# Performance work log

Hardware: AMD Instinct MI355X
Metric: run time of the kernel (lower is better)

Reference implementation:

```python
import jax, jax.numpy as jnp
import numpy as np

T, B, N, M, H, I = 64, 256, 256, 128, 1024, 128
S = 3  # 2*shift_range + 1
EPS = 1e-8  # torch cosine_similarity eps


def setup_inputs() -> dict:
    key = jax.random.key(0)
    ks = jax.random.split(key, 24)
    def rn(k, shp, scale):
        return (jax.random.normal(k, shp) * scale).astype(jnp.float32)
    sH = 1.0 / np.sqrt(H)
    sC = 1.0 / np.sqrt(I + M)
    sM = 1.0 / np.sqrt(M)
    return {
        'x': rn(ks[0], (T, B, I), 1.0),
        # controller (ffnn): Linear(I+M -> H), stored as [in, out]
        'Wc': rn(ks[1], (I + M, H), sC), 'bc': jnp.zeros((H,), jnp.float32),
        # head params stacked: index 0 = write head, 1 = read head
        'Wk': rn(ks[2], (2, H, M), sH), 'bk': jnp.zeros((2, M), jnp.float32),
        'Wb': rn(ks[3], (2, H, 1), sH), 'bb': jnp.zeros((2, 1), jnp.float32),
        'Wg': rn(ks[4], (2, H, 1), sH), 'bg': jnp.zeros((2, 1), jnp.float32),
        'Ws': rn(ks[5], (2, H, S), sH), 'bs': jnp.zeros((2, S), jnp.float32),
        'Wgam': rn(ks[6], (2, H, 1), sH), 'bgam': jnp.zeros((2, 1), jnp.float32),
        'We': rn(ks[7], (H, M), sH), 'be': jnp.zeros((M,), jnp.float32),
        'Wa': rn(ks[8], (H, M), sH), 'ba': rn(ks[9], (M,), 1.0),
        'Wo': rn(ks[10], (M, I), sM), 'bo': jnp.zeros((I,), jnp.float32),
        # learned initial state
        'memory0': rn(ks[11], (1, N, M), 0.05),
        'ww0': rn(ks[12], (1, N), 0.05),
        'rw0': rn(ks[13], (1, N), 0.05),
        'read0': rn(ks[14], (1, M), 0.05),
    }


def reference(x, Wc, bc, Wk, bk, Wb, bb, Wg, bg, Ws, bs, Wgam, bgam,
              We, be, Wa, ba, Wo, bo, memory0, ww0, rw0, read0):
    Bb = x.shape[1]
    Nn = memory0.shape[1]

    def head(i, ht, memory, prev_w):
        k = jax.nn.relu(ht @ Wk[i] + bk[i])                      # [B, M]
        beta = jax.nn.softplus(ht @ Wb[i] + bb[i])               # [B, 1]
        g = jax.nn.sigmoid(ht @ Wg[i] + bg[i])                   # [B, 1]
        shift = jax.nn.softmax(ht @ Ws[i] + bs[i], axis=1)       # [B, S]
        gamma = jax.nn.relu(ht @ Wgam[i] + bgam[i]) + 1.0        # [B, 1]
        # content addressing: cosine similarity then sharpened softmax
        kn = jnp.maximum(jnp.linalg.norm(k, axis=-1, keepdims=True), EPS)   # [B,1]
        mn = jnp.maximum(jnp.linalg.norm(memory, axis=-1), EPS)             # [B,N]
        cos = jnp.einsum('bm,bnm->bn', k, memory) / (kn * mn)
        w = jax.nn.softmax(beta * cos, axis=1)
        # interpolation with previous weight
        w = g * w + (1.0 - g) * prev_w
        # circular convolutional shift (kernel size S=3, cross-correlation like F.conv1d)
        pad = jnp.concatenate([w[:, -1:], w, w[:, :1]], axis=1)  # [B, N+2]
        w = sum(shift[:, j:j + 1] * pad[:, j:j + Nn] for j in range(S))
        # sharpening
        w = w ** gamma
        return w / jnp.sum(w, axis=1, keepdims=True)

    mem = jnp.tile(memory0, (Bb, 1, 1))
    ww = jax.nn.softmax(jnp.tile(ww0, (Bb, 1)), axis=1)
    rw = jax.nn.softmax(jnp.tile(rw0, (Bb, 1)), axis=1)
    rd = jnp.tile(read0, (Bb, 1))

    def step(carry, xt):
        memory, ww, rw, rd = carry
        inp = jnp.concatenate([xt, rd], axis=1)
        ht = jnp.tanh(inp @ Wc + bc)                             # ffnn controller
        ww = head(0, ht, memory, ww)                             # write head
        rw = head(1, ht, memory, rw)                             # read head
        erase = jax.nn.sigmoid(ht @ We + be)                     # [B, M]
        add = jax.nn.sigmoid(ht @ Wa + ba)                       # [B, M]
        memory = memory * (1.0 - ww[:, :, None] * erase[:, None, :]) \
                 + ww[:, :, None] * add[:, None, :]
        rd = jnp.einsum('bn,bnm->bm', rw, memory)
        out = rd @ Wo + bo
        return (memory, ww, rw, rd), out

    _, ys = jax.lax.scan(step, (mem, ww, rw, rd), x)
    return ys  # [T, B, I]
```

## Files before the change

kernel.cpp:

```cpp
#include <hip/hip_runtime.h>
#include <math.h>

#define T_ 64
#define B_ 256
#define N_ 256
#define M_ 128
#define H_ 1024
#define I_ 128
#define NB 256
#define NT 1024
#define MSTR 132
#define EPSF 1e-8f

#define WS_WCX 0
#define WS_WCR 65536
#define WS_W2P 131072
#define WS_WOP 393216
#define WS_WSM 401408
#define WS_XC  407552
#define WS_BYTES_NEEDED ((size_t)(407552 + 8388608) * 4)

typedef _Float16 h2_t __attribute__((ext_vector_type(2)));

__device__ __forceinline__ float fdot2(unsigned a, unsigned b, float c) {
  union { unsigned u; h2_t h; } ua, ub;
  ua.u = a; ub.u = b;
  return __builtin_amdgcn_fdot2(ua.h, ub.h, c, false);
}
__device__ __forceinline__ unsigned packh2(float a, float b) {
  union { h2_t h; unsigned u; } v;
  v.h = h2_t{(_Float16)a, (_Float16)b};
  return v.u;
}
__device__ __forceinline__ float dot4(uint4 w, uint4 h, float acc) {
  acc = fdot2(w.x, h.x, acc); acc = fdot2(w.y, h.y, acc);
  acc = fdot2(w.z, h.z, acc); acc = fdot2(w.w, h.w, acc);
  return acc;
}
__device__ __forceinline__ float wave_rsum(float v) {
#pragma unroll
  for (int o = 32; o > 0; o >>= 1) v += __shfl_xor(v, o, 64);
  return v;
}
__device__ __forceinline__ float wave_rmax(float v) {
#pragma unroll
  for (int o = 32; o > 0; o >>= 1) v = fmaxf(v, __shfl_xor(v, o, 64));
  return v;
}

__global__ void ntm_pack(const float* __restrict__ Wc, const float* __restrict__ Wk,
                         const float* __restrict__ Wb, const float* __restrict__ Wg,
                         const float* __restrict__ Wsf, const float* __restrict__ Wgm,
                         const float* __restrict__ We, const float* __restrict__ Wa,
                         const float* __restrict__ Wo,
                         unsigned* __restrict__ wsu)
{
  const int total = 407552;
  for (int i = blockIdx.x * blockDim.x + threadIdx.x; i < total;
       i += gridDim.x * blockDim.x) {
    if (i < 65536) {
      int jm = i & 3, q4 = i >> 2, k4 = q4 >> 10, h = q4 & 1023;
      int k0 = k4 * 8 + 2 * jm;
      wsu[WS_WCX + i] = packh2(Wc[(size_t)k0 * H_ + h], Wc[(size_t)(k0 + 1) * H_ + h]);
    } else if (i < 131072) {
      int u = i - 65536;
      int jm = u & 3, q4 = u >> 2, k4 = q4 >> 10, h = q4 & 1023;
      int k0 = 128 + k4 * 8 + 2 * jm;
      wsu[WS_WCR + u] = packh2(Wc[(size_t)k0 * H_ + h], Wc[(size_t)(k0 + 1) * H_ + h]);
    } else if (i < 393216) {
      int u = i - 131072;
      int jm = u & 3, q4 = u >> 2, k4 = q4 >> 9, c = q4 & 511;
      int k0 = k4 * 8 + 2 * jm, k1 = k0 + 1;
      float v0, v1;
      if (c < 128)      { v0 = Wk[(size_t)k0 * M_ + c];           v1 = Wk[(size_t)k1 * M_ + c]; }
      else if (c < 256) { v0 = Wk[(size_t)H_ * M_ + (size_t)k0 * M_ + (c - 128)];
                          v1 = Wk[(size_t)H_ * M_ + (size_t)k1 * M_ + (c - 128)]; }
      else if (c < 384) { v0 = We[(size_t)k0 * M_ + (c - 256)];   v1 = We[(size_t)k1 * M_ + (c - 256)]; }
      else              { v0 = Wa[(size_t)k0 * M_ + (c - 384)];   v1 = Wa[(size_t)k1 * M_ + (c - 384)]; }
      wsu[WS_W2P + u] = packh2(v0, v1);
    } else if (i < 401408) {
      int u = i - 393216;
      int jm = u & 3, q4 = u >> 2, k4 = q4 >> 7, c = q4 & 127;
      int m0 = k4 * 8 + 2 * jm;
      wsu[WS_WOP + u] = packh2(Wo[(size_t)m0 * I_ + c], Wo[(size_t)(m0 + 1) * I_ + c]);
    } else {
      int u = i - 401408, d = u >> 9, k2 = u & 511;
      int k0 = 2 * k2, k1 = 2 * k2 + 1;
      float v0, v1;
      if (d < 2)      { v0 = Wb[d * H_ + k0];        v1 = Wb[d * H_ + k1]; }
      else if (d < 4) { v0 = Wg[(d - 2) * H_ + k0];  v1 = Wg[(d - 2) * H_ + k1]; }
      else if (d < 6) { v0 = Wgm[(d - 4) * H_ + k0]; v1 = Wgm[(d - 4) * H_ + k1]; }
      else if (d < 9) { v0 = Wsf[k0 * 3 + (d - 6)];  v1 = Wsf[k1 * 3 + (d - 6)]; }
      else            { v0 = Wsf[3 * H_ + k0 * 3 + (d - 9)]; v1 = Wsf[3 * H_ + k1 * 3 + (d - 9)]; }
      wsu[WS_WSM + u] = packh2(v0, v1);
    }
  }
}

__global__ __launch_bounds__(256)
void ntm_xc(const float* __restrict__ x, const unsigned* __restrict__ wsu,
            unsigned* __restrict__ wsout)
{
  __shared__ __align__(16) _Float16 xt[16 * 128];
  const int tid = threadIdx.x;
  const size_t row0 = (size_t)blockIdx.x * 16;
  for (int i = tid; i < 16 * 128; i += 256)
    xt[i] = (_Float16)x[(row0 + (i >> 7)) * I_ + (i & 127)];
  __syncthreads();
  _Float16* xc16 = (_Float16*)(wsout + WS_XC);
  const uint4* xt4 = (const uint4*)xt;
  const uint4* w4 = (const uint4*)(wsu + WS_WCX);
  for (int cq = 0; cq < 4; ++cq) {
    const int col = cq * 256 + tid;
    float acc[16];
#pragma unroll
    for (int r = 0; r < 16; ++r) acc[r] = 0.f;
#pragma unroll 4
    for (int k4 = 0; k4 < 16; ++k4) {
      uint4 w = w4[k4 * 1024 + col];
#pragma unroll
      for (int r = 0; r < 16; ++r)
        acc[r] = dot4(w, xt4[r * 16 + k4], acc[r]);
    }
#pragma unroll
    for (int r = 0; r < 16; ++r)
      xc16[(row0 + r) * H_ + col] = (_Float16)acc[r];
  }
}

__global__ __launch_bounds__(NT)
void ntm_main(const float* __restrict__ x,
              const float* __restrict__ bc,  const float* __restrict__ bk,
              const float* __restrict__ bbv, const float* __restrict__ bg,
              const float* __restrict__ bsf, const float* __restrict__ bgm,
              const float* __restrict__ be,  const float* __restrict__ ba,
              const float* __restrict__ bo,
              const float* __restrict__ mem0, const float* __restrict__ ww0,
              const float* __restrict__ rw0,  const float* __restrict__ rd0,
              const unsigned* __restrict__ wsu,
              float* __restrict__ out, int useXc)
{
  __shared__ __align__(16) float mem[N_ * MSTR];
  __shared__ __align__(16) _Float16 ht16[H_];
  __shared__ __align__(16) _Float16 rd16[M_];
  __shared__ __align__(16) _Float16 x16[M_];
  __shared__ __align__(16) float prevw[2 * N_];
  __shared__ __align__(16) float mnv[N_];
  __shared__ __align__(16) float ksh[2 * M_];
  __shared__ __align__(16) float eah[2 * M_];
  __shared__ __align__(16) float wlog[2 * N_];
  __shared__ __align__(16) float wtmp[2 * N_];
  __shared__ __align__(16) float redU[2048];
  __shared__ __align__(16) float sdots[24];
  __shared__ __align__(16) float scal[32];
  __shared__ __align__(16) float bcL[H_];
  __shared__ __align__(16) float bkL[256];
  __shared__ __align__(16) float beL[128];
  __shared__ __align__(16) float baL[128];
  __shared__ __align__(16) float boL[128];
  __shared__ __align__(16) float sb[16];

  const int tid = threadIdx.x;
  const int b = blockIdx.x;
  const _Float16* xcg = (const _Float16*)(wsu + WS_XC);
  const uint4* wcx4 = (const uint4*)(wsu + WS_WCX);
  const uint4* wcr4 = (const uint4*)(wsu + WS_WCR);
  const uint4* w2p4 = (const uint4*)(wsu + WS_W2P);
  const uint4* wop4 = (const uint4*)(wsu + WS_WOP);
  const uint4* wsm4 = (const uint4*)(wsu + WS_WSM);
  const uint4* rp4 = (const uint4*)rd16;
  const uint4* hp4 = (const uint4*)ht16;

  for (int i = tid; i < N_ * M_; i += NT)
    mem[(i >> 7) * MSTR + (i & 127)] = mem0[i];
  bcL[tid] = bc[tid];
  if (tid < 256) bkL[tid] = bk[tid];
  if (tid < 128) { beL[tid] = be[tid]; baL[tid] = ba[tid]; boL[tid] = bo[tid]; }
  if (tid < 12) {
    float v;
    if (tid < 2) v = bbv[tid];
    else if (tid < 4) v = bg[tid - 2];
    else if (tid < 6) v = bgm[tid - 4];
    else v = bsf[tid - 6];
    sb[tid] = v;
  }
  if (tid < 512) wlog[tid] = (tid < 256) ? ww0[tid] : rw0[tid - 256];
  __syncthreads();
  if (tid < 256) {
    float s = 0.f;
#pragma unroll 8
    for (int m = 0; m < M_; ++m) { float v = mem[tid * MSTR + m]; s += v * v; }
    mnv[tid] = fmaxf(sqrtf(s), EPSF);
  }
  {
    int wv = tid >> 6, ln = tid & 63;
    if (wv < 2) {
      float l0 = wlog[wv * N_ + ln], l1 = wlog[wv * N_ + 64 + ln],
            l2 = wlog[wv * N_ + 128 + ln], l3 = wlog[wv * N_ + 192 + ln];
      float mx = wave_rmax(fmaxf(fmaxf(l0, l1), fmaxf(l2, l3)));
      float e0 = __expf(l0 - mx), e1 = __expf(l1 - mx), e2 = __expf(l2 - mx), e3 = __expf(l3 - mx);
      float sm = wave_rsum(e0 + e1 + e2 + e3);
      wlog[wv * N_ + ln] = e0; wlog[wv * N_ + 64 + ln] = e1;
      wlog[wv * N_ + 128 + ln] = e2; wlog[wv * N_ + 192 + ln] = e3;
      if (ln == 0) scal[30 + wv] = 1.f / sm;
    }
  }
  __syncthreads();
  if (tid < 512) prevw[tid] = wlog[tid] * scal[30 + (tid >> 8)];
  if (tid < 64)
    ((unsigned*)rd16)[tid] = packh2(rd0[2 * tid], rd0[2 * tid + 1]);
  if (!useXc && tid >= 64 && tid < 128) {
    int k = tid - 64;
    ((unsigned*)x16)[k] = packh2(x[(size_t)b * I_ + 2 * k], x[(size_t)b * I_ + 2 * k + 1]);
  }
  __syncthreads();

  for (int t = 0; t < T_; ++t) {
    {
      const int j = tid;
      float a0, a1 = 0.f;
      if (useXc) {
        a0 = (float)xcg[((size_t)t * B_ + b) * H_ + j];
      } else {
        a0 = 0.f;
        const uint4* xp4 = (const uint4*)x16;
#pragma unroll 4
        for (int k4 = 0; k4 < 16; k4 += 2) {
          a0 = dot4(wcx4[k4 * 1024 + j], xp4[k4], a0);
          a1 = dot4(wcx4[(k4 + 1) * 1024 + j], xp4[k4 + 1], a1);
        }
      }
#pragma unroll 4
      for (int k4 = 0; k4 < 16; k4 += 2) {
        a0 = dot4(wcr4[k4 * 1024 + j], rp4[k4], a0);
        a1 = dot4(wcr4[(k4 + 1) * 1024 + j], rp4[k4 + 1], a1);
      }
      ht16[j] = (_Float16)tanhf(a0 + a1 + bcL[j]);
      if (t > 0) {
        int c = tid & 127, q = tid >> 7;
        float s = dot4(wop4[(2 * q) * 128 + c], rp4[2 * q], 0.f);
        s = dot4(wop4[(2 * q + 1) * 128 + c], rp4[2 * q + 1], s);
        redU[1024 + q * 128 + c] = s;
      }
    }
    __syncthreads();

    {
      const int c = tid & 511, half = tid >> 9;
      const int kb = half * 64;
      float a0 = 0.f, a1 = 0.f, a2 = 0.f, a3 = 0.f;
#pragma unroll 8
      for (int k = 0; k < 64; k += 4) {
        a0 = dot4(w2p4[(kb + k) * 512 + c],     hp4[kb + k],     a0);
        a1 = dot4(w2p4[(kb + k + 1) * 512 + c], hp4[kb + k + 1], a1);
        a2 = dot4(w2p4[(kb + k + 2) * 512 + c], hp4[kb + k + 2], a2);
        a3 = dot4(w2p4[(kb + k + 3) * 512 + c], hp4[kb + k + 3], a3);
      }
      redU[half * 512 + c] = (a0 + a1) + (a2 + a3);
      if (tid < 128 && t > 0) {
        float o = boL[tid];
#pragma unroll
        for (int q = 0; q < 8; ++q) o += redU[1024 + q * 128 + tid];
        out[((size_t)(t - 1) * B_ + b) * I_ + tid] = o;
      }
    }
    __syncthreads();

    {
      if (tid < 512) {
        float v = redU[tid] + redU[512 + tid];
        if (tid < 256)      ksh[tid] = fmaxf(v + bkL[tid], 0.f);
        else if (tid < 384) eah[tid - 256] = 1.f / (1.f + __expf(-(v + beL[tid - 256])));
        else                eah[tid - 256] = 1.f / (1.f + __expf(-(v + baL[tid - 384])));
      } else {
        int wv = (tid >> 6) - 8, ln = tid & 63;
#pragma unroll
        for (int i = 0; i < 3; ++i) {
          int hd = wv * 3 + i;
          int d = hd >> 1, half = hd & 1;
          float s = dot4(wsm4[d * 128 + half * 64 + ln], hp4[half * 64 + ln], 0.f);
          s = wave_rsum(s);
          if (ln == 0) sdots[hd] = s;
        }
      }
    }
    __syncthreads();

    {
      if (tid == 0) {
        for (int h = 0; h < 2; ++h) {
          float Sb = sdots[2 * h] + sdots[2 * h + 1];
          float Sg = sdots[2 * (2 + h)] + sdots[2 * (2 + h) + 1];
          float Sgm = sdots[2 * (4 + h)] + sdots[2 * (4 + h) + 1];
          float rb = Sb + sb[h];
          scal[16 + h] = (rb > 20.f) ? rb : log1pf(__expf(rb));
          scal[18 + h] = 1.f / (1.f + __expf(-(Sg + sb[2 + h])));
          scal[20 + h] = fmaxf(Sgm + sb[4 + h], 0.f) + 1.f;
          float s0 = sdots[2 * (6 + 3 * h)] + sdots[2 * (6 + 3 * h) + 1] + sb[6 + 3 * h];
          float s1 = sdots[2 * (7 + 3 * h)] + sdots[2 * (7 + 3 * h) + 1] + sb[7 + 3 * h];
          float s2 = sdots[2 * (8 + 3 * h)] + sdots[2 * (8 + 3 * h) + 1] + sb[8 + 3 * h];
          float mx = fmaxf(s0, fmaxf(s1, s2));
          float e0 = __expf(s0 - mx), e1 = __expf(s1 - mx), e2 = __expf(s2 - mx);
          float inv = 1.f / (e0 + e1 + e2);
          scal[22 + 3 * h] = e0 * inv; scal[23 + 3 * h] = e1 * inv; scal[24 + 3 * h] = e2 * inv;
        }
      } else if (tid >= 64 && tid < 192) {
        int h = (tid >> 6) - 1, ln = tid & 63;
        float v0 = ksh[h * 128 + ln], v1 = ksh[h * 128 + 64 + ln];
        float s = wave_rsum(v0 * v0 + v1 * v1);
        if (ln == 0) scal[12 + h] = fmaxf(sqrtf(s), EPSF);
      }
    }
    __syncthreads();

    if (tid < 512) {
      int wv = tid >> 6, ln = tid & 63;
      int h = wv & 1, n = (wv >> 1) * 64 + ln;
      const float beta = scal[16 + h], kn = scal[12 + h];
      const float4* kp = (const float4*)&ksh[h * 128];
      const float* mrow = &mem[n * MSTR];
      float dot = 0.f;
#pragma unroll 8
      for (int m4 = 0; m4 < 32; ++m4) {
        float4 kv = kp[m4];
        float4 mv = *(const float4*)&mrow[m4 * 4];
        dot += kv.x * mv.x + kv.y * mv.y + kv.z * mv.z + kv.w * mv.w;
      }
      wlog[h * N_ + n] = beta * (dot / (kn * mnv[n]));
    }
    __syncthreads();

    {
      int wv = tid >> 6, ln = tid & 63;
      if (wv < 2) {
        float l0 = wlog[wv * N_ + ln], l1 = wlog[wv * N_ + 64 + ln],
              l2 = wlog[wv * N_ + 128 + ln], l3 = wlog[wv * N_ + 192 + ln];
        float mx = wave_rmax(fmaxf(fmaxf(l0, l1), fmaxf(l2, l3)));
        float e0 = __expf(l0 - mx), e1 = __expf(l1 - mx), e2 = __expf(l2 - mx), e3 = __expf(l3 - mx);
        float sm = wave_rsum(e0 + e1 + e2 + e3);
        wlog[wv * N_ + ln] = e0; wlog[wv * N_ + 64 + ln] = e1;
        wlog[wv * N_ + 128 + ln] = e2; wlog[wv * N_ + 192 + ln] = e3;
        if (ln == 0) scal[30 + wv] = 1.f / sm;
      }
    }
    __syncthreads();

    if (tid < 512) {
      int h = tid >> 8;
      float g = scal[18 + h];
      wtmp[tid] = g * wlog[tid] * scal[30 + h] + (1.f - g) * prevw[tid];
    }
    __syncthreads();

    if (tid < 512) {
      int h = tid >> 8, n = tid & 255;
      float v = scal[22 + 3 * h] * wtmp[h * N_ + ((n + 255) & 255)]
              + scal[23 + 3 * h] * wtmp[h * N_ + n]
              + scal[24 + 3 * h] * wtmp[h * N_ + ((n + 1) & 255)];
      wlog[tid] = __powf(v, scal[20 + h]);
    }
    __syncthreads();

    {
      int wv = tid >> 6, ln = tid & 63;
      if (wv < 2) {
        float s = wlog[wv * N_ + ln] + wlog[wv * N_ + 64 + ln]
                + wlog[wv * N_ + 128 + ln] + wlog[wv * N_ + 192 + ln];
        s = wave_rsum(s);
        if (ln == 0) scal[14 + wv] = 1.f / s;
      }
    }
    __syncthreads();

    {
      int n = tid & 255, q = tid >> 8;
      float wwn = wlog[n] * scal[14];
      float* mrow = &mem[n * MSTR + q * 32];
      const float4* ep = (const float4*)&eah[q * 32];
      const float4* ap = (const float4*)&eah[128 + q * 32];
      float sq = 0.f;
#pragma unroll
      for (int i = 0; i < 8; ++i) {
        float4 mv = *(float4*)&mrow[i * 4];
        float4 ev = ep[i], av = ap[i];
        mv.x = mv.x * (1.f - wwn * ev.x) + wwn * av.x;
        mv.y = mv.y * (1.f - wwn * ev.y) + wwn * av.y;
        mv.z = mv.z * (1.f - wwn * ev.z) + wwn * av.z;
        mv.w = mv.w * (1.f - wwn * ev.w) + wwn * av.w;
        sq += mv.x * mv.x + mv.y * mv.y + mv.z * mv.z + mv.w * mv.w;
        *(float4*)&mrow[i * 4] = mv;
      }
      redU[1024 + q * 256 + n] = sq;
      if (q == 0) prevw[n] = wwn;
    }
    __syncthreads();

    {
      int m = tid & 127, g = tid >> 7;
      const float* basep = &mem[g * 32 * MSTR + m];
      float acc = 0.f;
#pragma unroll 8
      for (int i = 0; i < 32; ++i)
        acc += wlog[256 + g * 32 + i] * basep[i * MSTR];
      redU[g * 128 + m] = acc;
    }
    __syncthreads();

    {
      if (tid < 64) {
        float r0 = 0.f, r1 = 0.f;
#pragma unroll
        for (int g = 0; g < 8; ++g) {
          r0 += redU[g * 128 + 2 * tid];
          r1 += redU[g * 128 + 2 * tid + 1];
        }
        ((unsigned*)rd16)[tid] = packh2(r0 * scal[15], r1 * scal[15]);
      } else if (tid >= 256 && tid < 512) {
        int n = tid - 256;
        prevw[256 + n] = wlog[256 + n] * scal[15];
      } else if (tid >= 512 && tid < 768) {
        int n = tid - 512;
        float s = redU[1024 + n] + redU[1280 + n] + redU[1536 + n] + redU[1792 + n];
        mnv[n] = fmaxf(sqrtf(s), EPSF);
      } else if (!useXc && tid >= 768 && tid < 832 && t < T_ - 1) {
        int k = tid - 768;
        const float* xr = &x[((size_t)(t + 1) * B_ + b) * I_];
        ((unsigned*)x16)[k] = packh2(xr[2 * k], xr[2 * k + 1]);
      }
    }
    __syncthreads();
  }

  {
    int c = tid & 127, q = tid >> 7;
    float s = dot4(wop4[(2 * q) * 128 + c], rp4[2 * q], 0.f);
    s = dot4(wop4[(2 * q + 1) * 128 + c], rp4[2 * q + 1], s);
    redU[1024 + q * 128 + c] = s;
  }
  __syncthreads();
  if (tid < 128) {
    float o = boL[tid];
#pragma unroll
    for (int q = 0; q < 8; ++q) o += redU[1024 + q * 128 + tid];
    out[((size_t)(T_ - 1) * B_ + b) * I_ + tid] = o;
  }
}

extern "C" void kernel_launch(void* const* d_in, const int* in_sizes, int n_in,
                              void* d_out, int out_size, void* d_ws, size_t ws_size,
                              hipStream_t stream) {
  (void)in_sizes; (void)n_in; (void)out_size;

  const float* x    = (const float*)d_in[0];
  const float* Wc   = (const float*)d_in[1];
  const float* bc   = (const float*)d_in[2];
  const float* Wk   = (const float*)d_in[3];
  const float* bk   = (const float*)d_in[4];
  const float* Wb   = (const float*)d_in[5];
  const float* bbv  = (const float*)d_in[6];
  const float* Wg   = (const float*)d_in[7];
  const float* bg   = (const float*)d_in[8];
  const float* Wsf  = (const float*)d_in[9];
  const float* bsf  = (const float*)d_in[10];
  const float* Wgm  = (const float*)d_in[11];
  const float* bgm  = (const float*)d_in[12];
  const float* We   = (const float*)d_in[13];
  const float* be   = (const float*)d_in[14];
  const float* Wa   = (const float*)d_in[15];
  const float* ba   = (const float*)d_in[16];
  const float* Wo   = (const float*)d_in[17];
  const float* bo   = (const float*)d_in[18];
  const float* mem0 = (const float*)d_in[19];
  const float* ww0  = (const float*)d_in[20];
  const float* rw0  = (const float*)d_in[21];
  const float* rd0  = (const float*)d_in[22];
  float* out = (float*)d_out;
  unsigned* wsu = (unsigned*)d_ws;

  const int useXc = (ws_size >= WS_BYTES_NEEDED) ? 1 : 0;

  ntm_pack<<<dim3(512), dim3(256), 0, stream>>>(Wc, Wk, Wb, Wg, Wsf, Wgm, We, Wa, Wo, wsu);
  if (useXc)
    ntm_xc<<<dim3(T_ * B_ / 16), dim3(256), 0, stream>>>(x, wsu, wsu);
  ntm_main<<<dim3(NB), dim3(NT), 0, stream>>>(x, bc, bk, bbv, bg, bsf, bgm, be, ba, bo,
                                              mem0, ww0, rw0, rd0, wsu, out, useXc);
}
```

Before: 1.375 ms.

## Fuse per-step head addressing phases into fewer barriers with wave-level shuffles

Restructures the per-timestep pipeline to cut the number of block-wide barriers. The split-K head projection now reduces in registers with a cross-lane shuffle and applies the activations in place. The key norm moves into the cosine-similarity pass. The beta/gate/shift/gamma scalars, softmax, interpolation, circular shift, sharpening and normalisation all run inside two waves using shuffles instead of several separate phases. It also software-pipelines the weight loads in the controller and head GEMVs, vectorises the read-vector accumulation, and moves the memory-norm computation into an earlier phase. The trade-off is that one wave per head serialises the addressing math, and the extra shuffles and register prefetching may raise register pressure.

```diff
diff --git a/kernel.cpp b/kernel.cpp
--- a/kernel.cpp
+++ b/kernel.cpp
@@ -218,7 +218,7 @@
   for (int t = 0; t < T_; ++t) {
     {
       const int j = tid;
-      float a0, a1 = 0.f;
+      float a0, a1 = 0.f, a2 = 0.f, a3 = 0.f;
       if (useXc) {
         a0 = (float)xcg[((size_t)t * B_ + b) * H_ + j];
       } else {
@@ -230,151 +230,142 @@
           a1 = dot4(wcx4[(k4 + 1) * 1024 + j], xp4[k4 + 1], a1);
         }
       }
-#pragma unroll 4
-      for (int k4 = 0; k4 < 16; k4 += 2) {
-        a0 = dot4(wcr4[k4 * 1024 + j], rp4[k4], a0);
-        a1 = dot4(wcr4[(k4 + 1) * 1024 + j], rp4[k4 + 1], a1);
-      }
-      ht16[j] = (_Float16)tanhf(a0 + a1 + bcL[j]);
-      if (t > 0) {
+      uint4 p0 = wcr4[0 * 1024 + j], p1 = wcr4[1 * 1024 + j],
+            p2 = wcr4[2 * 1024 + j], p3 = wcr4[3 * 1024 + j];
+      for (int k4 = 0; k4 < 12; k4 += 4) {
+        uint4 t0 = p0, t1 = p1, t2 = p2, t3 = p3;
+        p0 = wcr4[(k4 + 4) * 1024 + j]; p1 = wcr4[(k4 + 5) * 1024 + j];
+        p2 = wcr4[(k4 + 6) * 1024 + j]; p3 = wcr4[(k4 + 7) * 1024 + j];
+        a0 = dot4(t0, rp4[k4], a0);     a1 = dot4(t1, rp4[k4 + 1], a1);
+        a2 = dot4(t2, rp4[k4 + 2], a2); a3 = dot4(t3, rp4[k4 + 3], a3);
+      }
+      a0 = dot4(p0, rp4[12], a0); a1 = dot4(p1, rp4[13], a1);
+      a2 = dot4(p2, rp4[14], a2); a3 = dot4(p3, rp4[15], a3);
+      ht16[j] = (_Float16)tanhf(((a0 + a1) + (a2 + a3)) + bcL[j]);
+      if (tid < 512) {
         int c = tid & 127, q = tid >> 7;
-        float s = dot4(wop4[(2 * q) * 128 + c], rp4[2 * q], 0.f);
-        s = dot4(wop4[(2 * q + 1) * 128 + c], rp4[2 * q + 1], s);
-        redU[1024 + q * 128 + c] = s;
+        float s = 0.f;
+#pragma unroll
+        for (int i = 0; i < 4; ++i)
+          s = dot4(wop4[(q * 4 + i) * 128 + c], rp4[q * 4 + i], s);
+        wtmp[q * 128 + c] = s;
       }
     }
     __syncthreads();
 
     {
-      const int c = tid & 511, half = tid >> 9;
-      const int kb = half * 64;
+      const int w = tid >> 6, l = tid & 63;
+      const int c = w * 32 + (l & 31);
+      const int kk = (l >> 5) * 64;
+      uint4 b0 = w2p4[(size_t)(kk + 0) * 512 + c], b1 = w2p4[(size_t)(kk + 1) * 512 + c],
+            b2 = w2p4[(size_t)(kk + 2) * 512 + c], b3 = w2p4[(size_t)(kk + 3) * 512 + c];
       float a0 = 0.f, a1 = 0.f, a2 = 0.f, a3 = 0.f;
-#pragma unroll 8
-      for (int k = 0; k < 64; k += 4) {
-        a0 = dot4(w2p4[(kb + k) * 512 + c],     hp4[kb + k],     a0);
-        a1 = dot4(w2p4[(kb + k + 1) * 512 + c], hp4[kb + k + 1], a1);
-        a2 = dot4(w2p4[(kb + k + 2) * 512 + c], hp4[kb + k + 2], a2);
-        a3 = dot4(w2p4[(kb + k + 3) * 512 + c], hp4[kb + k + 3], a3);
-      }
-      redU[half * 512 + c] = (a0 + a1) + (a2 + a3);
+      for (int k = 0; k < 60; k += 4) {
+        uint4 t0 = b0, t1 = b1, t2 = b2, t3 = b3;
+        b0 = w2p4[(size_t)(kk + k + 4) * 512 + c]; b1 = w2p4[(size_t)(kk + k + 5) * 512 + c];
+        b2 = w2p4[(size_t)(kk + k + 6) * 512 + c]; b3 = w2p4[(size_t)(kk + k + 7) * 512 + c];
+        a0 = dot4(t0, hp4[kk + k], a0);     a1 = dot4(t1, hp4[kk + k + 1], a1);
+        a2 = dot4(t2, hp4[kk + k + 2], a2); a3 = dot4(t3, hp4[kk + k + 3], a3);
+      }
+      a0 = dot4(b0, hp4[kk + 60], a0); a1 = dot4(b1, hp4[kk + 61], a1);
+      a2 = dot4(b2, hp4[kk + 62], a2); a3 = dot4(b3, hp4[kk + 63], a3);
+      float acc = (a0 + a1) + (a2 + a3);
+      acc += __shfl_xor(acc, 32, 64);
+      if (l < 32) {
+        if (c < 256)      ksh[c] = fmaxf(acc + bkL[c], 0.f);
+        else if (c < 384) eah[c - 256] = 1.f / (1.f + __expf(-(acc + beL[c - 256])));
+        else              eah[c - 256] = 1.f / (1.f + __expf(-(acc + baL[c - 384])));
+      }
+      if (w >= 10) {
+#pragma unroll
+        for (int i = 0; i < 4; ++i) {
+          int hd = (w - 10) * 4 + i;
+          int d = hd >> 1, half = hd & 1;
+          float s = dot4(wsm4[d * 128 + half * 64 + l], hp4[half * 64 + l], 0.f);
+          s = wave_rsum(s);
+          if (l == 0) sdots[hd] = s;
+        }
+      }
       if (tid < 128 && t > 0) {
-        float o = boL[tid];
-#pragma unroll
-        for (int q = 0; q < 8; ++q) o += redU[1024 + q * 128 + tid];
+        float o = boL[tid] + wtmp[tid] + wtmp[128 + tid] + wtmp[256 + tid] + wtmp[384 + tid];
         out[((size_t)(t - 1) * B_ + b) * I_ + tid] = o;
       }
-    }
-    __syncthreads();
-
-    {
-      if (tid < 512) {
-        float v = redU[tid] + redU[512 + tid];
-        if (tid < 256)      ksh[tid] = fmaxf(v + bkL[tid], 0.f);
-        else if (tid < 384) eah[tid - 256] = 1.f / (1.f + __expf(-(v + beL[tid - 256])));
-        else                eah[tid - 256] = 1.f / (1.f + __expf(-(v + baL[tid - 384])));
-      } else {
-        int wv = (tid >> 6) - 8, ln = tid & 63;
-#pragma unroll
-        for (int i = 0; i < 3; ++i) {
-          int hd = wv * 3 + i;
-          int d = hd >> 1, half = hd & 1;
-          float s = dot4(wsm4[d * 128 + half * 64 + ln], hp4[half * 64 + ln], 0.f);
-          s = wave_rsum(s);
-          if (ln == 0) sdots[hd] = s;
-        }
-      }
-    }
-    __syncthreads();
-
-    {
-      if (tid == 0) {
-        for (int h = 0; h < 2; ++h) {
-          float Sb = sdots[2 * h] + sdots[2 * h + 1];
-          float Sg = sdots[2 * (2 + h)] + sdots[2 * (2 + h) + 1];
-          float Sgm = sdots[2 * (4 + h)] + sdots[2 * (4 + h) + 1];
-          float rb = Sb + sb[h];
-          scal[16 + h] = (rb > 20.f) ? rb : log1pf(__expf(rb));
-          scal[18 + h] = 1.f / (1.f + __expf(-(Sg + sb[2 + h])));
-          scal[20 + h] = fmaxf(Sgm + sb[4 + h], 0.f) + 1.f;
-          float s0 = sdots[2 * (6 + 3 * h)] + sdots[2 * (6 + 3 * h) + 1] + sb[6 + 3 * h];
-          float s1 = sdots[2 * (7 + 3 * h)] + sdots[2 * (7 + 3 * h) + 1] + sb[7 + 3 * h];
-          float s2 = sdots[2 * (8 + 3 * h)] + sdots[2 * (8 + 3 * h) + 1] + sb[8 + 3 * h];
-          float mx = fmaxf(s0, fmaxf(s1, s2));
-          float e0 = __expf(s0 - mx), e1 = __expf(s1 - mx), e2 = __expf(s2 - mx);
-          float inv = 1.f / (e0 + e1 + e2);
-          scal[22 + 3 * h] = e0 * inv; scal[23 + 3 * h] = e1 * inv; scal[24 + 3 * h] = e2 * inv;
-        }
-      } else if (tid >= 64 && tid < 192) {
-        int h = (tid >> 6) - 1, ln = tid & 63;
-        float v0 = ksh[h * 128 + ln], v1 = ksh[h * 128 + 64 + ln];
-        float s = wave_rsum(v0 * v0 + v1 * v1);
-        if (ln == 0) scal[12 + h] = fmaxf(sqrtf(s), EPSF);
-      }
-    }
-    __syncthreads();
-
-    if (tid < 512) {
-      int wv = tid >> 6, ln = tid & 63;
-      int h = wv & 1, n = (wv >> 1) * 64 + ln;
-      const float beta = scal[16 + h], kn = scal[12 + h];
-      const float4* kp = (const float4*)&ksh[h * 128];
-      const float* mrow = &mem[n * MSTR];
-      float dot = 0.f;
-#pragma unroll 8
-      for (int m4 = 0; m4 < 32; ++m4) {
-        float4 kv = kp[m4];
-        float4 mv = *(const float4*)&mrow[m4 * 4];
-        dot += kv.x * mv.x + kv.y * mv.y + kv.z * mv.z + kv.w * mv.w;
-      }
-      wlog[h * N_ + n] = beta * (dot / (kn * mnv[n]));
     }
     __syncthreads();
 
     {
       int wv = tid >> 6, ln = tid & 63;
-      if (wv < 2) {
-        float l0 = wlog[wv * N_ + ln], l1 = wlog[wv * N_ + 64 + ln],
-              l2 = wlog[wv * N_ + 128 + ln], l3 = wlog[wv * N_ + 192 + ln];
-        float mx = wave_rmax(fmaxf(fmaxf(l0, l1), fmaxf(l2, l3)));
-        float e0 = __expf(l0 - mx), e1 = __expf(l1 - mx), e2 = __expf(l2 - mx), e3 = __expf(l3 - mx);
-        float sm = wave_rsum(e0 + e1 + e2 + e3);
-        wlog[wv * N_ + ln] = e0; wlog[wv * N_ + 64 + ln] = e1;
-        wlog[wv * N_ + 128 + ln] = e2; wlog[wv * N_ + 192 + ln] = e3;
-        if (ln == 0) scal[30 + wv] = 1.f / sm;
-      }
-    }
-    __syncthreads();
-
-    if (tid < 512) {
-      int h = tid >> 8;
-      float g = scal[18 + h];
-      wtmp[tid] = g * wlog[tid] * scal[30 + h] + (1.f - g) * prevw[tid];
-    }
-    __syncthreads();
-
-    if (tid < 512) {
-      int h = tid >> 8, n = tid & 255;
-      float v = scal[22 + 3 * h] * wtmp[h * N_ + ((n + 255) & 255)]
-              + scal[23 + 3 * h] * wtmp[h * N_ + n]
-              + scal[24 + 3 * h] * wtmp[h * N_ + ((n + 1) & 255)];
-      wlog[tid] = __powf(v, scal[20 + h]);
-    }
-    __syncthreads();
-
-    {
-      int wv = tid >> 6, ln = tid & 63;
-      if (wv < 2) {
-        float s = wlog[wv * N_ + ln] + wlog[wv * N_ + 64 + ln]
-                + wlog[wv * N_ + 128 + ln] + wlog[wv * N_ + 192 + ln];
-        s = wave_rsum(s);
-        if (ln == 0) scal[14 + wv] = 1.f / s;
-      }
+      int h = wv & 1, nblk = wv >> 1;
+      int r = nblk * 32 + (ln & 31), mh = ln >> 5;
+      const float4* kp = (const float4*)&ksh[h * 128 + mh * 64];
+      const float* mrow = &mem[r * MSTR + mh * 64];
+      float dot = 0.f, kq = 0.f;
+#pragma unroll
+      for (int i = 0; i < 16; ++i) {
+        float4 kv = kp[i];
+        float4 mv = *(const float4*)&mrow[i * 4];
+        dot += kv.x * mv.x + kv.y * mv.y + kv.z * mv.z + kv.w * mv.w;
+        kq  += kv.x * kv.x + kv.y * kv.y + kv.z * kv.z + kv.w * kv.w;
+      }
+      dot += __shfl_xor(dot, 32, 64);
+      kq  += __shfl_xor(kq, 32, 64);
+      if (ln < 32) {
+        float kn = fmaxf(sqrtf(kq), EPSF);
+        wlog[h * N_ + r] = dot / (kn * mnv[r]);
+      }
+    }
+    __syncthreads();
+
+    if (tid < 128) {
+      int h = tid >> 6, ln = tid & 63;
+      float Sb = sdots[2 * h] + sdots[2 * h + 1] + sb[h];
+      float beta = (Sb > 20.f) ? Sb : log1pf(__expf(Sb));
+      float g = 1.f / (1.f + __expf(-(sdots[2 * (2 + h)] + sdots[2 * (2 + h) + 1] + sb[2 + h])));
+      float gam = fmaxf(sdots[2 * (4 + h)] + sdots[2 * (4 + h) + 1] + sb[4 + h], 0.f) + 1.f;
+      float t0 = sdots[2 * (6 + 3 * h)] + sdots[2 * (6 + 3 * h) + 1] + sb[6 + 3 * h];
+      float t1 = sdots[2 * (7 + 3 * h)] + sdots[2 * (7 + 3 * h) + 1] + sb[7 + 3 * h];
+      float t2 = sdots[2 * (8 + 3 * h)] + sdots[2 * (8 + 3 * h) + 1] + sb[8 + 3 * h];
+      float mx3 = fmaxf(t0, fmaxf(t1, t2));
+      float e0s = __expf(t0 - mx3), e1s = __expf(t1 - mx3), e2s = __expf(t2 - mx3);
+      float inv3 = 1.f / (e0s + e1s + e2s);
+      float s0 = e0s * inv3, s1 = e1s * inv3, s2 = e2s * inv3;
+      float w0 = beta * wlog[h * N_ + ln],        w1 = beta * wlog[h * N_ + 64 + ln];
+      float w2 = beta * wlog[h * N_ + 128 + ln],  w3 = beta * wlog[h * N_ + 192 + ln];
+      float mx = wave_rmax(fmaxf(fmaxf(w0, w1), fmaxf(w2, w3)));
+      w0 = __expf(w0 - mx); w1 = __expf(w1 - mx); w2 = __expf(w2 - mx); w3 = __expf(w3 - mx);
+      float inv = 1.f / wave_rsum(w0 + w1 + w2 + w3);
+      w0 = g * w0 * inv + (1.f - g) * prevw[h * N_ + ln];
+      w1 = g * w1 * inv + (1.f - g) * prevw[h * N_ + 64 + ln];
+      w2 = g * w2 * inv + (1.f - g) * prevw[h * N_ + 128 + ln];
+      w3 = g * w3 * inv + (1.f - g) * prevw[h * N_ + 192 + ln];
+      int lm = (ln + 63) & 63, lp = (ln + 1) & 63;
+      float l0 = __shfl(w0, lm, 64), l1 = __shfl(w1, lm, 64),
+            l2 = __shfl(w2, lm, 64), l3 = __shfl(w3, lm, 64);
+      float e0 = __shfl(w0, 63, 64), e1 = __shfl(w1, 63, 64),
+            e2 = __shfl(w2, 63, 64), e3 = __shfl(w3, 63, 64);
+      if (ln == 0) { l0 = e3; l1 = e0; l2 = e1; l3 = e2; }
+      float r0 = __shfl(w0, lp, 64), r1 = __shfl(w1, lp, 64),
+            r2 = __shfl(w2, lp, 64), r3 = __shfl(w3, lp, 64);
+      float f0 = __shfl(w0, 0, 64), f1 = __shfl(w1, 0, 64),
+            f2 = __shfl(w2, 0, 64), f3 = __shfl(w3, 0, 64);
+      if (ln == 63) { r0 = f1; r1 = f2; r2 = f3; r3 = f0; }
+      float u0 = s0 * l0 + s1 * w0 + s2 * r0;
+      float u1 = s0 * l1 + s1 * w1 + s2 * r1;
+      float u2 = s0 * l2 + s1 * w2 + s2 * r2;
+      float u3 = s0 * l3 + s1 * w3 + s2 * r3;
+      u0 = __powf(u0, gam); u1 = __powf(u1, gam);
+      u2 = __powf(u2, gam); u3 = __powf(u3, gam);
+      float invs = 1.f / wave_rsum(u0 + u1 + u2 + u3);
+      prevw[h * N_ + ln] = u0 * invs;
+      prevw[h * N_ + 64 + ln] = u1 * invs;
+      prevw[h * N_ + 128 + ln] = u2 * invs;
+      prevw[h * N_ + 192 + ln] = u3 * invs;
     }
     __syncthreads();
 
     {
       int n = tid & 255, q = tid >> 8;
-      float wwn = wlog[n] * scal[14];
+      float wwn = prevw[n];
       float* mrow = &mem[n * MSTR + q * 32];
       const float4* ep = (const float4*)&eah[q * 32];
       const float4* ap = (const float4*)&eah[128 + q * 32];
@@ -391,18 +382,24 @@
         *(float4*)&mrow[i * 4] = mv;
       }
       redU[1024 + q * 256 + n] = sq;
-      if (q == 0) prevw[n] = wwn;
-    }
-    __syncthreads();
-
-    {
-      int m = tid & 127, g = tid >> 7;
-      const float* basep = &mem[g * 32 * MSTR + m];
-      float acc = 0.f;
+    }
+    __syncthreads();
+
+    if (tid < 256) {
+      int m4 = tid & 31, g = tid >> 5;
+      const float* base = &mem[(g * 32) * MSTR + m4 * 4];
+      float4 acc = {0.f, 0.f, 0.f, 0.f};
 #pragma unroll 8
-      for (int i = 0; i < 32; ++i)
-        acc += wlog[256 + g * 32 + i] * basep[i * MSTR];
-      redU[g * 128 + m] = acc;
+      for (int i = 0; i < 32; ++i) {
+        float rw = prevw[256 + g * 32 + i];
+        float4 mv = *(const float4*)&base[i * MSTR];
+        acc.x += rw * mv.x; acc.y += rw * mv.y; acc.z += rw * mv.z; acc.w += rw * mv.w;
+      }
+      *(float4*)&redU[g * 128 + m4 * 4] = acc;
+    } else if (tid >= 512 && tid < 768) {
+      int n = tid - 512;
+      float s = redU[1024 + n] + redU[1280 + n] + redU[1536 + n] + redU[1792 + n];
+      mnv[n] = fmaxf(sqrtf(s), EPSF);
     }
     __syncthreads();
 
@@ -414,14 +411,7 @@
           r0 += redU[g * 128 + 2 * tid];
           r1 += redU[g * 128 + 2 * tid + 1];
         }
-        ((unsigned*)rd16)[tid] = packh2(r0 * scal[15], r1 * scal[15]);
-      } else if (tid >= 256 && tid < 512) {
-        int n = tid - 256;
-        prevw[256 + n] = wlog[256 + n] * scal[15];
-      } else if (tid >= 512 && tid < 768) {
-        int n = tid - 512;
-        float s = redU[1024 + n] + redU[1280 + n] + redU[1536 + n] + redU[1792 + n];
-        mnv[n] = fmaxf(sqrtf(s), EPSF);
+        ((unsigned*)rd16)[tid] = packh2(r0, r1);
       } else if (!useXc && tid >= 768 && tid < 832 && t < T_ - 1) {
         int k = tid - 768;
         const float* xr = &x[((size_t)(t + 1) * B_ + b) * I_];
@@ -431,17 +421,17 @@
     __syncthreads();
   }
 
-  {
+  if (tid < 512) {
     int c = tid & 127, q = tid >> 7;
-    float s = dot4(wop4[(2 * q) * 128 + c], rp4[2 * q], 0.f);
-    s = dot4(wop4[(2 * q + 1) * 128 + c], rp4[2 * q + 1], s);
-    redU[1024 + q * 128 + c] = s;
+    float s = 0.f;
+#pragma unroll
+    for (int i = 0; i < 4; ++i)
+      s = dot4(wop4[(q * 4 + i) * 128 + c], rp4[q * 4 + i], s);
+    wtmp[q * 128 + c] = s;
   }
   __syncthreads();
   if (tid < 128) {
-    float o = boL[tid];
-#pragma unroll
-    for (int q = 0; q < 8; ++q) o += redU[1024 + q * 128 + tid];
+    float o = boL[tid] + wtmp[tid] + wtmp[128 + tid] + wtmp[256 + tid] + wtmp[384 + tid];
     out[((size_t)(T_ - 1) * B_ + b) * I_ + tid] = o;
   }
 }
```

After: 4.597 ms. +234.4%, slower.
